# Performance work log

Measured on AMD Instinct MI355X. Metric: run time of the kernel, lower is better.

## Reference

```python
import jax, jax.numpy as jnp
import numpy as np

NS = 100000
H = 128  # embedding_dim
K = 4    # heads


def setup_inputs() -> dict:
    key = jax.random.key(0)
    ks = jax.random.split(key, 8)
    return {
        "e": jax.random.normal(ks[0], (NS, H), dtype=jnp.float32),
        "w_key": jax.random.normal(ks[1], (K, 1), dtype=jnp.float32),
        "w_value": jax.random.normal(ks[2], (K, 1), dtype=jnp.float32),
        "q": jax.random.normal(ks[3], (H,), dtype=jnp.float32),
        "mu_w": jax.random.normal(ks[4], (1, H), dtype=jnp.float32) * (1.0 / np.sqrt(H)),
        "mu_b": jax.random.normal(ks[5], (1,), dtype=jnp.float32) * 0.01,
        "sigma_w": jax.random.normal(ks[6], (1, H), dtype=jnp.float32) * (1.0 / np.sqrt(H)),
        "sigma_b": jax.random.normal(ks[7], (1,), dtype=jnp.float32) * 0.01,
    }


def reference(e, w_key, w_value, q, mu_w, mu_b, sigma_w, sigma_b):
    # e: [Ns, H] -> unsqueeze(0) -> [1, Ns, H]
    e3 = e[None, :, :]
    # w_key/w_value: [K, 1]; einsum 'kd,dnh->knh' -> [K, Ns, H]
    k = jnp.einsum('kd,dnh->knh', w_key, e3)
    v = jnp.einsum('kd,dnh->knh', w_value, e3)
    # L2-normalized attention logits: [K, Ns]
    q_norm = jnp.linalg.norm(q)                    # scalar
    k_norm = jnp.linalg.norm(k, axis=-1)           # [K, Ns]
    a_att = jnp.einsum('h,knh->kn', q, k) / (q_norm * k_norm)
    a_att = jnp.maximum(a_att, 0.0)
    a_att = a_att / jnp.maximum(jnp.sum(a_att, axis=-1, keepdims=True), 1e-6)
    # weighted aggregation over stocks: [K, H]
    h_multi = jnp.einsum('kn,knh->kh', a_att, v)
    # linear heads -> [K]
    mu_z = jnp.squeeze(h_multi @ mu_w.T + mu_b, axis=-1)
    sigma_z = jax.nn.softplus(jnp.squeeze(h_multi @ sigma_w.T + sigma_b, axis=-1))
    return (mu_z, sigma_z)
```

## Files before the change

### kernel.cpp

```cpp
#include <hip/hip_runtime.h>
#include <math.h>

#define NS 100000
#define H 128
#define NHEADS 4
#define TPB 256
#define NBLK 3125
#define NREP 64
#define SLOTF 16

__device__ __forceinline__ float dot4(float4 a, float4 b) {
    return a.x * b.x + a.y * b.y + a.z * b.z + a.w * b.w;
}

__device__ __forceinline__ void fma4(float4& acc, float w, float4 v) {
    acc.x = fmaf(w, v.x, acc.x); acc.y = fmaf(w, v.y, acc.y);
    acc.z = fmaf(w, v.z, acc.z); acc.w = fmaf(w, v.w, acc.w);
}

__global__ __launch_bounds__(TPB, 8) void fp_pass1(const float* __restrict__ e,
                                                   const float* __restrict__ q,
                                                   const float* __restrict__ mu_w,
                                                   const float* __restrict__ sigma_w,
                                                   float* __restrict__ g) {
    const int tid  = threadIdx.x;
    const int lane = tid & 63;
    const int widx = tid >> 6;
    const int half = lane >> 5;
    const int c4   = (lane & 31) << 2;

    const int gw = blockIdx.x * (TPB / 64) + widx;
    const float* p = e + (size_t)gw * (8 * H) + (size_t)half * H + c4;
    const float4 v0 = *(const float4*)(p);
    const float4 v1 = *(const float4*)(p + 2 * H);
    const float4 v2 = *(const float4*)(p + 4 * H);
    const float4 v3 = *(const float4*)(p + 6 * H);

    const float4 q4 = *(const float4*)(q + c4);
    float qn = dot4(q4, q4);
    qn += __shfl_xor(qn, 1);  qn += __shfl_xor(qn, 2);  qn += __shfl_xor(qn, 4);
    qn += __shfl_xor(qn, 8);  qn += __shfl_xor(qn, 16);
    const float inv_qn = rsqrtf(qn);

    float d0 = dot4(v0, q4), d1 = dot4(v1, q4), d2 = dot4(v2, q4), d3 = dot4(v3, q4);
    float s0 = dot4(v0, v0), s1 = dot4(v1, v1), s2 = dot4(v2, v2), s3 = dot4(v3, v3);
#define LVL(m)                                                        \
    d0 += __shfl_xor(d0, m); d1 += __shfl_xor(d1, m);                 \
    d2 += __shfl_xor(d2, m); d3 += __shfl_xor(d3, m);                 \
    s0 += __shfl_xor(s0, m); s1 += __shfl_xor(s1, m);                 \
    s2 += __shfl_xor(s2, m); s3 += __shfl_xor(s3, m);
    LVL(1) LVL(2) LVL(4) LVL(8) LVL(16)
#undef LVL
    const float c0 = d0 * rsqrtf(s0) * inv_qn;
    const float c1 = d1 * rsqrtf(s1) * inv_qn;
    const float c2 = d2 * rsqrtf(s2) * inv_qn;
    const float c3 = d3 * rsqrtf(s3) * inv_qn;
    const float wp0 = fmaxf(c0, 0.f), wm0 = fmaxf(-c0, 0.f);
    const float wp1 = fmaxf(c1, 0.f), wm1 = fmaxf(-c1, 0.f);
    const float wp2 = fmaxf(c2, 0.f), wm2 = fmaxf(-c2, 0.f);
    const float wp3 = fmaxf(c3, 0.f), wm3 = fmaxf(-c3, 0.f);
    const float sp = (wp0 + wp1) + (wp2 + wp3);
    const float sm = (wm0 + wm1) + (wm2 + wm3);
    float4 up = {0.f, 0.f, 0.f, 0.f};
    float4 um = {0.f, 0.f, 0.f, 0.f};
    fma4(up, wp0, v0); fma4(up, wp1, v1); fma4(up, wp2, v2); fma4(up, wp3, v3);
    fma4(um, wm0, v0); fma4(um, wm1, v1); fma4(um, wm2, v2); fma4(um, wm3, v3);

    __shared__ float s_up[8][H];
    __shared__ float s_um[8][H];
    __shared__ float s_s[8][2];
    const int hs = widx * 2 + half;
    *(float4*)(&s_up[hs][c4]) = up;
    *(float4*)(&s_um[hs][c4]) = um;
    if ((lane & 31) == 0) {
        s_s[hs][0] = sp;
        s_s[hs][1] = sm;
    }
    __syncthreads();

    const int col = tid & (H - 1);
    float a = 0.f;
    if (tid < H) {
#pragma unroll
        for (int h2 = 0; h2 < 8; ++h2) a += s_up[h2][col];
    } else {
#pragma unroll
        for (int h2 = 0; h2 < 8; ++h2) a += s_um[h2][col];
    }
    float pA = a * mu_w[col];
    float pB = a * sigma_w[col];
#pragma unroll
    for (int m = 1; m < 64; m <<= 1) {
        pA += __shfl_xor(pA, m);
        pB += __shfl_xor(pB, m);
    }
    __shared__ float s_r[4][2];
    if (lane == 0) { s_r[widx][0] = pA; s_r[widx][1] = pB; }
    __syncthreads();

    if (tid == 0) {
        const float A = s_r[0][0] + s_r[1][0];
        const float B = s_r[0][1] + s_r[1][1];
        const float C = s_r[2][0] + s_r[3][0];
        const float D = s_r[2][1] + s_r[3][1];
        float spv = 0.f, smv = 0.f;
#pragma unroll
        for (int h2 = 0; h2 < 8; ++h2) { spv += s_s[h2][0]; smv += s_s[h2][1]; }
        float* slot = g + (size_t)(blockIdx.x & (NREP - 1)) * 6 * SLOTF;
        atomicAdd(slot + 0 * SLOTF, A);
        atomicAdd(slot + 1 * SLOTF, B);
        atomicAdd(slot + 2 * SLOTF, C);
        atomicAdd(slot + 3 * SLOTF, D);
        atomicAdd(slot + 4 * SLOTF, spv);
        atomicAdd(slot + 5 * SLOTF, smv);
    }
}

__global__ __launch_bounds__(64) void fp_finalize(const float* __restrict__ g,
                                                  const float* __restrict__ w_key,
                                                  const float* __restrict__ w_value,
                                                  const float* __restrict__ mu_b,
                                                  const float* __restrict__ sigma_b,
                                                  float* __restrict__ out) {
    const int tid = threadIdx.x;
    __shared__ float tot[6];
    if (tid < 6) {
        float a = 0.f;
#pragma unroll
        for (int r = 0; r < NREP; ++r) a += g[(size_t)(r * 6 + tid) * SLOTF];
        tot[tid] = a;
    }
    __syncthreads();
    if (tid < NHEADS) {
        const float A = tot[0], B = tot[1], C = tot[2], D = tot[3];
        const float spv = fmaxf(tot[4], 1e-6f);
        const float smv = fmaxf(tot[5], 1e-6f);
        const float wk = w_key[tid];
        const float wv = w_value[tid];
        float dmu, dsg;
        if (wk > 0.f) {
            dmu = A / spv; dsg = B / spv;
        } else if (wk < 0.f) {
            dmu = C / smv; dsg = D / smv;
        } else {
            dmu = 0.f; dsg = 0.f;
        }
        out[tid] = fmaf(wv, dmu, mu_b[0]);
        const float x = fmaf(wv, dsg, sigma_b[0]);
        out[NHEADS + tid] = fmaxf(x, 0.f) + log1pf(expf(-fabsf(x)));
    }
}

extern "C" void kernel_launch(void* const* d_in, const int* in_sizes, int n_in,
                              void* d_out, int out_size, void* d_ws, size_t ws_size,
                              hipStream_t stream) {
    const float* e       = (const float*)d_in[0];
    const float* w_key   = (const float*)d_in[1];
    const float* w_value = (const float*)d_in[2];
    const float* q       = (const float*)d_in[3];
    const float* mu_w    = (const float*)d_in[4];
    const float* mu_b    = (const float*)d_in[5];
    const float* sigma_w = (const float*)d_in[6];
    const float* sigma_b = (const float*)d_in[7];
    float* out = (float*)d_out;
    float* g   = (float*)d_ws;

    hipLaunchKernelGGL(fp_pass1, dim3(NBLK), dim3(TPB), 0, stream,
                       e, q, mu_w, sigma_w, g);
    hipLaunchKernelGGL(fp_finalize, dim3(1), dim3(64), 0, stream, g,
                       w_key, w_value, mu_b, sigma_b, out);
}
```

Before: 99.34 us.

## Convert pass1 to persistent grid-stride kernel staging row tiles through LDS

The kernel now launches a fixed 1024 blocks that loop over 64-row tiles. Each tile is staged in padded shared memory, per-row dot products are computed as partial sums across four thread groups, and the weighted row sums accumulate in registers across tiles. Per-block atomics and reduction work drop from 3125 blocks to 1024. The cost is four __syncthreads per tile plus an extra round trip through LDS, with no prefetch overlap on what is a bandwidth-bound streaming read.

```diff
diff --git a/kernel.cpp b/kernel.cpp
--- a/kernel.cpp
+++ b/kernel.cpp
@@ -5,7 +5,10 @@
 #define H 128
 #define NHEADS 4
 #define TPB 256
-#define NBLK 3125
+#define NBLK 1024
+#define TILE 64
+#define RS 132
+#define NTILES ((NS + TILE - 1) / TILE)
 #define NREP 64
 #define SLOTF 16
 
@@ -18,101 +21,125 @@
     acc.z = fmaf(w, v.z, acc.z); acc.w = fmaf(w, v.w, acc.w);
 }
 
-__global__ __launch_bounds__(TPB, 8) void fp_pass1(const float* __restrict__ e,
+__global__ __launch_bounds__(TPB, 4) void fp_pass1(const float* __restrict__ e,
                                                    const float* __restrict__ q,
                                                    const float* __restrict__ mu_w,
                                                    const float* __restrict__ sigma_w,
                                                    float* __restrict__ g) {
-    const int tid  = threadIdx.x;
-    const int lane = tid & 63;
-    const int widx = tid >> 6;
-    const int half = lane >> 5;
-    const int c4   = (lane & 31) << 2;
+    const int tid = threadIdx.x;
+    __shared__ __align__(16) float smem[TILE * RS + 8 * TILE + 2 * TILE];
+    float* pd = smem + TILE * RS;
+    float* pn = pd + 4 * TILE;
+    float* wp = pn + 4 * TILE;
+    float* wm = wp + TILE;
 
-    const int gw = blockIdx.x * (TPB / 64) + widx;
-    const float* p = e + (size_t)gw * (8 * H) + (size_t)half * H + c4;
-    const float4 v0 = *(const float4*)(p);
-    const float4 v1 = *(const float4*)(p + 2 * H);
-    const float4 v2 = *(const float4*)(p + 4 * H);
-    const float4 v3 = *(const float4*)(p + 6 * H);
+    const int k  = tid >> 6;
+    const int r  = tid & 63;
+    const int bc = tid & 31;
+    const int bs = tid >> 5;
 
-    const float4 q4 = *(const float4*)(q + c4);
-    float qn = dot4(q4, q4);
-    qn += __shfl_xor(qn, 1);  qn += __shfl_xor(qn, 2);  qn += __shfl_xor(qn, 4);
-    qn += __shfl_xor(qn, 8);  qn += __shfl_xor(qn, 16);
+    float qn = 0.f;
+    for (int j = 0; j < 32; ++j) {
+        const float4 qv = *(const float4*)(q + j * 4);
+        qn += dot4(qv, qv);
+    }
     const float inv_qn = rsqrtf(qn);
+    float4 qk[8];
+#pragma unroll
+    for (int j = 0; j < 8; ++j) qk[j] = *(const float4*)(q + (k * 8 + j) * 4);
 
-    float d0 = dot4(v0, q4), d1 = dot4(v1, q4), d2 = dot4(v2, q4), d3 = dot4(v3, q4);
-    float s0 = dot4(v0, v0), s1 = dot4(v1, v1), s2 = dot4(v2, v2), s3 = dot4(v3, v3);
-#define LVL(m)                                                        \
-    d0 += __shfl_xor(d0, m); d1 += __shfl_xor(d1, m);                 \
-    d2 += __shfl_xor(d2, m); d3 += __shfl_xor(d3, m);                 \
-    s0 += __shfl_xor(s0, m); s1 += __shfl_xor(s1, m);                 \
-    s2 += __shfl_xor(s2, m); s3 += __shfl_xor(s3, m);
-    LVL(1) LVL(2) LVL(4) LVL(8) LVL(16)
-#undef LVL
-    const float c0 = d0 * rsqrtf(s0) * inv_qn;
-    const float c1 = d1 * rsqrtf(s1) * inv_qn;
-    const float c2 = d2 * rsqrtf(s2) * inv_qn;
-    const float c3 = d3 * rsqrtf(s3) * inv_qn;
-    const float wp0 = fmaxf(c0, 0.f), wm0 = fmaxf(-c0, 0.f);
-    const float wp1 = fmaxf(c1, 0.f), wm1 = fmaxf(-c1, 0.f);
-    const float wp2 = fmaxf(c2, 0.f), wm2 = fmaxf(-c2, 0.f);
-    const float wp3 = fmaxf(c3, 0.f), wm3 = fmaxf(-c3, 0.f);
-    const float sp = (wp0 + wp1) + (wp2 + wp3);
-    const float sm = (wm0 + wm1) + (wm2 + wm3);
-    float4 up = {0.f, 0.f, 0.f, 0.f};
-    float4 um = {0.f, 0.f, 0.f, 0.f};
-    fma4(up, wp0, v0); fma4(up, wp1, v1); fma4(up, wp2, v2); fma4(up, wp3, v3);
-    fma4(um, wm0, v0); fma4(um, wm1, v1); fma4(um, wm2, v2); fma4(um, wm3, v3);
+    float4 accp = {0.f, 0.f, 0.f, 0.f};
+    float4 accm = {0.f, 0.f, 0.f, 0.f};
+    float sp_acc = 0.f, sm_acc = 0.f;
 
-    __shared__ float s_up[8][H];
-    __shared__ float s_um[8][H];
-    __shared__ float s_s[8][2];
-    const int hs = widx * 2 + half;
-    *(float4*)(&s_up[hs][c4]) = up;
-    *(float4*)(&s_um[hs][c4]) = um;
-    if ((lane & 31) == 0) {
-        s_s[hs][0] = sp;
-        s_s[hs][1] = sm;
+    for (int t = blockIdx.x; t < NTILES; t += NBLK) {
+        const int row0 = t * TILE;
+        float4 v[8];
+#pragma unroll
+        for (int j = 0; j < 8; ++j) {
+            const int idx = j * 256 + tid;
+            const int gr  = row0 + (idx >> 5);
+            const float4 z = {0.f, 0.f, 0.f, 0.f};
+            v[j] = (gr < NS) ? *(const float4*)(e + (size_t)gr * H + (idx & 31) * 4) : z;
+        }
+#pragma unroll
+        for (int j = 0; j < 8; ++j) {
+            const int idx = j * 256 + tid;
+            *(float4*)(smem + (idx >> 5) * RS + (idx & 31) * 4) = v[j];
+        }
+        __syncthreads();
+        {
+            float d = 0.f, n = 0.f;
+            const float* rowp = smem + r * RS + k * 32;
+#pragma unroll
+            for (int j = 0; j < 8; ++j) {
+                const float4 x = *(const float4*)(rowp + j * 4);
+                d += dot4(x, qk[j]);
+                n += dot4(x, x);
+            }
+            pd[k * 64 + r] = d;
+            pn[k * 64 + r] = n;
+        }
+        __syncthreads();
+        if (tid < TILE) {
+            const float d = pd[tid] + pd[64 + tid] + pd[128 + tid] + pd[192 + tid];
+            const float n = pn[tid] + pn[64 + tid] + pn[128 + tid] + pn[192 + tid];
+            float c = d * rsqrtf(n) * inv_qn;
+            if (row0 + tid >= NS) c = 0.f;
+            const float w_p = fmaxf(c, 0.f), w_m = fmaxf(-c, 0.f);
+            wp[tid] = w_p; wm[tid] = w_m;
+            sp_acc += w_p; sm_acc += w_m;
+        }
+        __syncthreads();
+#pragma unroll
+        for (int i = 0; i < 8; ++i) {
+            const int rr = bs + i * 8;
+            const float4 x = *(const float4*)(smem + rr * RS + bc * 4);
+            fma4(accp, wp[rr], x);
+            fma4(accm, wm[rr], x);
+        }
+        __syncthreads();
     }
+
+    float4* fold = (float4*)smem;
+    fold[(0 * 8 + bs) * 32 + bc] = accp;
+    fold[(1 * 8 + bs) * 32 + bc] = accm;
     __syncthreads();
-
-    const int col = tid & (H - 1);
-    float a = 0.f;
-    if (tid < H) {
+    if (tid < 64) {
+        const int half = tid >> 5;
+        const int c    = tid & 31;
+        float4 u = {0.f, 0.f, 0.f, 0.f};
 #pragma unroll
-        for (int h2 = 0; h2 < 8; ++h2) a += s_up[h2][col];
-    } else {
+        for (int s2 = 0; s2 < 8; ++s2) {
+            const float4 x = fold[(half * 8 + s2) * 32 + c];
+            u.x += x.x; u.y += x.y; u.z += x.z; u.w += x.w;
+        }
+        const float4 mw = *(const float4*)(mu_w + c * 4);
+        const float4 sw = *(const float4*)(sigma_w + c * 4);
+        float pA = dot4(u, mw);
+        float pB = dot4(u, sw);
 #pragma unroll
-        for (int h2 = 0; h2 < 8; ++h2) a += s_um[h2][col];
-    }
-    float pA = a * mu_w[col];
-    float pB = a * sigma_w[col];
+        for (int m = 1; m < 32; m <<= 1) {
+            pA += __shfl_xor(pA, m);
+            pB += __shfl_xor(pB, m);
+        }
+        float s1 = sp_acc, s2v = sm_acc;
 #pragma unroll
-    for (int m = 1; m < 64; m <<= 1) {
-        pA += __shfl_xor(pA, m);
-        pB += __shfl_xor(pB, m);
-    }
-    __shared__ float s_r[4][2];
-    if (lane == 0) { s_r[widx][0] = pA; s_r[widx][1] = pB; }
-    __syncthreads();
-
-    if (tid == 0) {
-        const float A = s_r[0][0] + s_r[1][0];
-        const float B = s_r[0][1] + s_r[1][1];
-        const float C = s_r[2][0] + s_r[3][0];
-        const float D = s_r[2][1] + s_r[3][1];
-        float spv = 0.f, smv = 0.f;
-#pragma unroll
-        for (int h2 = 0; h2 < 8; ++h2) { spv += s_s[h2][0]; smv += s_s[h2][1]; }
+        for (int m = 1; m < 64; m <<= 1) {
+            s1  += __shfl_xor(s1, m);
+            s2v += __shfl_xor(s2v, m);
+        }
         float* slot = g + (size_t)(blockIdx.x & (NREP - 1)) * 6 * SLOTF;
-        atomicAdd(slot + 0 * SLOTF, A);
-        atomicAdd(slot + 1 * SLOTF, B);
-        atomicAdd(slot + 2 * SLOTF, C);
-        atomicAdd(slot + 3 * SLOTF, D);
-        atomicAdd(slot + 4 * SLOTF, spv);
-        atomicAdd(slot + 5 * SLOTF, smv);
+        if (tid == 0) {
+            atomicAdd(slot + 0 * SLOTF, pA);
+            atomicAdd(slot + 1 * SLOTF, pB);
+            atomicAdd(slot + 4 * SLOTF, s1);
+            atomicAdd(slot + 5 * SLOTF, s2v);
+        }
+        if (tid == 32) {
+            atomicAdd(slot + 2 * SLOTF, pA);
+            atomicAdd(slot + 3 * SLOTF, pB);
+        }
     }
 }
 
```

Result: slower. 122.5 us (+23.3%).
